# Kernel optimization log

Measured on AMD Instinct MI355X. Metric: run time of the kernel, lower is better.

## Reference

```python
import jax, jax.numpy as jnp
import numpy as np

N = 4096
M0 = 2048
M1 = 2048
MCS = 4096
STRIDE = 2
D_NNGP = STRIDE ** 2 * M1              # 8192, input dim of layer-1 arccos maps
D_NTK = STRIDE ** 2 * (MCS + M1)       # 24576, input dim1 of layer-1 count sketch


def setup_inputs() -> dict:
    key = jax.random.key(0)
    ks = jax.random.split(key, 8)
    return {
        "layer_idx": 1,
        "z_nngp": jax.random.normal(ks[0], (N, D_NNGP), jnp.float32),
        "z_ntk": jax.random.normal(ks[1], (N, D_NTK), jnp.float32),
        "W0": jax.random.normal(ks[2], (D_NNGP, M0), jnp.float32),   # arccos0[1].W
        "W1": jax.random.normal(ks[3], (D_NNGP, M1), jnp.float32),   # arccos1[1].W
        "sign1": (jax.random.randint(ks[4], (D_NTK,), 0, 2) * 2 - 1).astype(jnp.float32),
        "indx1": jax.random.randint(ks[5], (D_NTK,), 0, MCS),
        "sign2": (jax.random.randint(ks[6], (M0,), 0, 2) * 2 - 1).astype(jnp.float32),
        "indx2": jax.random.randint(ks[7], (M0,), 0, MCS),
    }


def count_sketch(x, indx, sign, out_dim):
    # x: [n, d_in]; sign-multiply then scatter_add along last axis into out_dim bins
    xs = x * sign[None, :]
    out = jnp.zeros((x.shape[0], out_dim), dtype=x.dtype)
    return out.at[:, indx].add(xs)


def reference(layer_idx, z_nngp, z_ntk, W0, W1, sign1, indx1, sign2, indx2):
    norm0 = np.sqrt(2.0 / M0).astype(np.float32)
    norm1 = np.float32(np.sqrt(2.0 / M1) / 2.0)
    # arccos order-0 feature map (step function)
    xw0 = z_nngp @ W0
    tmp = (xw0 > 0).astype(z_nngp.dtype) * norm0          # [N, M0]
    # arccos order-1 feature map (relu-like: |xw| + xw)
    xw1 = z_nngp @ W1
    z_nngp_out = (jnp.abs(xw1) + xw1) * norm1             # [N, M1]
    # tensor sketch: count-sketch both, FFT, complex pointwise multiply, ifft.real
    x_cs = count_sketch(z_ntk, indx1, sign1, MCS)         # [N, MCS]
    y_cs = count_sketch(tmp, indx2, sign2, MCS)           # [N, MCS]
    z_ntk_out = jnp.fft.ifft(jnp.fft.fft(x_cs, axis=-1) * jnp.fft.fft(y_cs, axis=-1)).real
    z_ntk_cat = jnp.concatenate([z_nngp_out, z_ntk_out], axis=1)  # [N, M1+MCS]
    return (z_nngp_out, z_ntk_cat)
```

## Files before the change

### kernel.cpp

```cpp
#include <hip/hip_runtime.h>

#define NROW 4096
#define KDIM 8192
#define MDIM 2048
#define MCS_ 4096
#define DNTK 24576
#define CATW 6144
#define TAU_HALF 2.5e-3f
#define NT (KDIM / 32)

typedef __attribute__((ext_vector_type(8))) short short8;
typedef __attribute__((ext_vector_type(4))) float f32x4;

__device__ __forceinline__ void split2(float x0, float x1,
                                       unsigned& hi, unsigned& lo) {
    const unsigned u0 = __float_as_uint(x0);
    const unsigned u1 = __float_as_uint(x1);
    hi = (u0 >> 16) | (u1 & 0xFFFF0000u);
    const float l0 = x0 - __uint_as_float(u0 & 0xFFFF0000u);
    const float l1 = x1 - __uint_as_float(u1 & 0xFFFF0000u);
    lo = (__float_as_uint(l0) >> 16) | (__float_as_uint(l1) & 0xFFFF0000u);
}

__device__ __forceinline__ float2 cmulf(float2 a, float2 b) {
    return make_float2(a.x * b.x - a.y * b.y, a.x * b.y + a.y * b.x);
}

__global__ __launch_bounds__(512) void convert_kernel(
    const float* __restrict__ A,
    const float* __restrict__ W1,
    const float* __restrict__ W0,
    short8* __restrict__ aHi, short8* __restrict__ aLo,
    short8* __restrict__ wHi, short8* __restrict__ wLo)
{
    int b = blockIdx.x;
    const int tid = threadIdx.x;
    if (b < 4096) {
        const int P = b >> 8, T = b & 255;
        const float* src = A + (size_t)(P * 256) * KDIM + T * 32;
        short8* dh = aHi + ((size_t)b << 10);
        short8* dl = aLo + ((size_t)b << 10);
        for (int s = tid; s < 1024; s += 512) {
            const int row = ((s >> 6) << 4) | (s & 15);
            const int k0  = ((s >> 4) & 3) * 8;
            const float* p = src + (size_t)row * KDIM + k0;
            const float4 v0 = *reinterpret_cast<const float4*>(p);
            const float4 v1 = *reinterpret_cast<const float4*>(p + 4);
            union { short8 ss; unsigned u[4]; } h, l;
            split2(v0.x, v0.y, h.u[0], l.u[0]);
            split2(v0.z, v0.w, h.u[1], l.u[1]);
            split2(v1.x, v1.y, h.u[2], l.u[2]);
            split2(v1.z, v1.w, h.u[3], l.u[3]);
            dh[s] = h.ss; dl[s] = l.ss;
        }
    } else {
        b -= 4096;
        const int mat = b >> 11;
        const int T   = b & 255;
        const int Pc  = (b >> 8) & 7;
        const float* Wm = mat ? W0 : W1;
        const float* src = Wm + (size_t)(T * 32) * MDIM + Pc * 256;
        short8* dh = wHi + ((size_t)b << 10);
        short8* dl = wLo + ((size_t)b << 10);
        for (int s = tid; s < 1024; s += 512) {
            const int col = ((s >> 6) << 4) | (s & 15);
            const int k0  = ((s >> 4) & 3) * 8;
            float v[8];
#pragma unroll
            for (int j = 0; j < 8; ++j)
                v[j] = src[(size_t)(k0 + j) * MDIM + col];
            union { short8 ss; unsigned u[4]; } h, l;
            split2(v[0], v[1], h.u[0], l.u[0]);
            split2(v[2], v[3], h.u[1], l.u[1]);
            split2(v[4], v[5], h.u[2], l.u[2]);
            split2(v[6], v[7], h.u[3], l.u[3]);
            dh[s] = h.ss; dl[s] = l.ss;
        }
    }
}

__global__ __launch_bounds__(512, 2) void gemm_mfma_pre(
    const short8* __restrict__ aHi, const short8* __restrict__ aLo,
    const short8* __restrict__ wHi, const short8* __restrict__ wLo,
    float* __restrict__ out0, float* __restrict__ outCat)
{
    const int mode = blockIdx.z;
    __shared__ short8 AhiS[2][1024], AloS[2][1024];
    __shared__ short8 BhiS[2][1024], BloS[2][1024];

    const int tid  = threadIdx.x;
    const int lane = tid & 63;
    const int wid  = tid >> 6;
    const int wr   = wid >> 1;
    const int wc   = wid & 1;
    const int brow = blockIdx.y * 256;
    const int bcol = blockIdx.x * 256;

    const size_t aBase = ((size_t)blockIdx.y) << 18;
    const size_t wBase = ((size_t)(mode * 8 + blockIdx.x)) << 18;

    f32x4 acc[4][8];
#pragma unroll
    for (int m = 0; m < 4; ++m)
#pragma unroll
        for (int n = 0; n < 8; ++n)
#pragma unroll
            for (int i = 0; i < 4; ++i) acc[m][n][i] = 0.f;

    short8 st[8];

#define ISSUE(T)                                                             \
    {                                                                        \
        const size_t o = ((size_t)(T)) << 10;                                \
        st[0] = aHi[aBase + o + tid];  st[1] = aHi[aBase + o + tid + 512];   \
        st[2] = aLo[aBase + o + tid];  st[3] = aLo[aBase + o + tid + 512];   \
        st[4] = wHi[wBase + o + tid];  st[5] = wHi[wBase + o + tid + 512];   \
        st[6] = wLo[wBase + o + tid];  st[7] = wLo[wBase + o + tid + 512];   \
    }
#define WRITE(BUF)                                                           \
    {                                                                        \
        AhiS[BUF][tid] = st[0];  AhiS[BUF][tid + 512] = st[1];               \
        AloS[BUF][tid] = st[2];  AloS[BUF][tid + 512] = st[3];               \
        BhiS[BUF][tid] = st[4];  BhiS[BUF][tid + 512] = st[5];               \
        BloS[BUF][tid] = st[6];  BloS[BUF][tid + 512] = st[7];               \
    }

    ISSUE(0); WRITE(0); ISSUE(1);
    __syncthreads();

    for (int t = 0; t < NT; ++t) {
        const int cur = t & 1;

        short8 ah[4], al[4];
#pragma unroll
        for (int m = 0; m < 4; ++m) {
            ah[m] = AhiS[cur][(wr * 4 + m) * 64 + lane];
            al[m] = AloS[cur][(wr * 4 + m) * 64 + lane];
        }

        if (t + 1 < NT) {
            WRITE(cur ^ 1);
            if (t + 2 < NT) ISSUE(t + 2);
        }

#pragma unroll
        for (int n = 0; n < 8; ++n) {
            const short8 bh = BhiS[cur][(wc * 8 + n) * 64 + lane];
            const short8 bl = BloS[cur][(wc * 8 + n) * 64 + lane];
#pragma unroll
            for (int m = 0; m < 4; ++m) {
                acc[m][n] = __builtin_amdgcn_mfma_f32_16x16x32_bf16(
                    ah[m], bh, acc[m][n], 0, 0, 0);
                acc[m][n] = __builtin_amdgcn_mfma_f32_16x16x32_bf16(
                    ah[m], bl, acc[m][n], 0, 0, 0);
                acc[m][n] = __builtin_amdgcn_mfma_f32_16x16x32_bf16(
                    al[m], bh, acc[m][n], 0, 0, 0);
            }
        }
        __syncthreads();
    }
#undef ISSUE
#undef WRITE

    const float norm0 = 0.03125f;
    const int ocol0 = bcol + wc * 128 + (lane & 15);
    const int orow0 = brow + wr * 64 + ((lane >> 4) << 2);
#pragma unroll
    for (int m = 0; m < 4; ++m)
#pragma unroll
        for (int n = 0; n < 8; ++n) {
            const int col = ocol0 + n * 16;
#pragma unroll
            for (int i = 0; i < 4; ++i) {
                const int row = orow0 + m * 16 + i;
                if (mode == 0) {
                    const float v = fmaxf(acc[m][n][i], 0.f) * norm0;
                    out0[(size_t)row * MDIM + col] = v;
                    outCat[(size_t)row * CATW + col] = v;
                } else {
                    outCat[(size_t)row * CATW + 2048 + col] = acc[m][n][i];
                }
            }
        }
}

__global__ __launch_bounds__(512, 2) void gemm_mfma(
    const float* __restrict__ A,
    const float* __restrict__ W1,
    const float* __restrict__ W0,
    float* __restrict__ out0,
    float* __restrict__ outCat)
{
    const int mode = blockIdx.z;
    const float* __restrict__ W = mode ? W0 : W1;

    __shared__ short8 AhiS[2][1024], AloS[2][1024];
    __shared__ short8 BhiS[2][1024], BloS[2][1024];

    const int tid  = threadIdx.x;
    const int lane = tid & 63;
    const int wid  = tid >> 6;
    const int wr   = wid >> 1;
    const int wc   = wid & 1;
    const int brow = blockIdx.y * 256;
    const int bcol = blockIdx.x * 256;

    f32x4 acc[4][8];
#pragma unroll
    for (int m = 0; m < 4; ++m)
#pragma unroll
        for (int n = 0; n < 8; ++n)
#pragma unroll
            for (int i = 0; i < 4; ++i) acc[m][n][i] = 0.f;

    const int srow  = tid >> 1;
    const int skh   = tid & 1;
    const int slot0 = (srow >> 4) * 64 + (srow & 15) + (skh << 5);
    const float* aptr = A + (size_t)(brow + srow) * KDIM + skh * 16;
    const float* bptr = W + (size_t)(skh * 16) * MDIM + (bcol + srow);

    float4 av0, av1, av2, av3;
    float  bst[16];

#define LOAD_TILE(T)                                                         \
    {                                                                        \
        const float* ap = aptr + (T) * 32;                                   \
        av0 = *reinterpret_cast<const float4*>(ap);                          \
        av1 = *reinterpret_cast<const float4*>(ap + 4);                      \
        av2 = *reinterpret_cast<const float4*>(ap + 8);                      \
        av3 = *reinterpret_cast<const float4*>(ap + 12);                     \
        const float* bp = bptr + (size_t)((T) * 32) * MDIM;                  \
        _Pragma("unroll")                                                    \
        for (int j = 0; j < 16; ++j) bst[j] = bp[(size_t)j * MDIM];          \
    }
#define CONVERT_WRITE(BUF)                                                   \
    {                                                                        \
        union { short8 s; unsigned u[4]; } h, l;                             \
        split2(av0.x, av0.y, h.u[0], l.u[0]);                                \
        split2(av0.z, av0.w, h.u[1], l.u[1]);                                \
        split2(av1.x, av1.y, h.u[2], l.u[2]);                                \
        split2(av1.z, av1.w, h.u[3], l.u[3]);                                \
        AhiS[BUF][slot0] = h.s;  AloS[BUF][slot0] = l.s;                     \
        split2(av2.x, av2.y, h.u[0], l.u[0]);                                \
        split2(av2.z, av2.w, h.u[1], l.u[1]);                                \
        split2(av3.x, av3.y, h.u[2], l.u[2]);                                \
        split2(av3.z, av3.w, h.u[3], l.u[3]);                                \
        AhiS[BUF][slot0 + 16] = h.s;  AloS[BUF][slot0 + 16] = l.s;           \
        split2(bst[0], bst[1], h.u[0], l.u[0]);                              \
        split2(bst[2], bst[3], h.u[1], l.u[1]);                              \
        split2(bst[4], bst[5], h.u[2], l.u[2]);                              \
        split2(bst[6], bst[7], h.u[3], l.u[3]);                              \
        BhiS[BUF][slot0] = h.s;  BloS[BUF][slot0] = l.s;                     \
        split2(bst[8],  bst[9],  h.u[0], l.u[0]);                            \
        split2(bst[10], bst[11], h.u[1], l.u[1]);                            \
        split2(bst[12], bst[13], h.u[2], l.u[2]);                            \
        split2(bst[14], bst[15], h.u[3], l.u[3]);                            \
        BhiS[BUF][slot0 + 16] = h.s;  BloS[BUF][slot0 + 16] = l.s;           \
    }

    LOAD_TILE(0);
    CONVERT_WRITE(0);
    LOAD_TILE(1);
    __syncthreads();

    for (int t = 0; t < NT; ++t) {
        const int cur = t & 1;
        short8 ah[4], al[4];
#pragma unroll
        for (int m = 0; m < 4; ++m) {
            ah[m] = AhiS[cur][(wr * 4 + m) * 64 + lane];
            al[m] = AloS[cur][(wr * 4 + m) * 64 + lane];
        }
        if (t + 1 < NT) {
            CONVERT_WRITE(cur ^ 1);
            if (t + 2 < NT) LOAD_TILE(t + 2);
        }
#pragma unroll
        for (int n = 0; n < 8; ++n) {
            const short8 bh = BhiS[cur][(wc * 8 + n) * 64 + lane];
            const short8 bl = BloS[cur][(wc * 8 + n) * 64 + lane];
#pragma unroll
            for (int m = 0; m < 4; ++m) {
                acc[m][n] = __builtin_amdgcn_mfma_f32_16x16x32_bf16(
                    ah[m], bh, acc[m][n], 0, 0, 0);
                acc[m][n] = __builtin_amdgcn_mfma_f32_16x16x32_bf16(
                    ah[m], bl, acc[m][n], 0, 0, 0);
                acc[m][n] = __builtin_amdgcn_mfma_f32_16x16x32_bf16(
                    al[m], bh, acc[m][n], 0, 0, 0);
            }
        }
        __syncthreads();
    }
#undef LOAD_TILE
#undef CONVERT_WRITE

    const float norm0 = 0.03125f;
    const int ocol0 = bcol + wc * 128 + (lane & 15);
    const int orow0 = brow + wr * 64 + ((lane >> 4) << 2);
#pragma unroll
    for (int m = 0; m < 4; ++m)
#pragma unroll
        for (int n = 0; n < 8; ++n) {
            const int col = ocol0 + n * 16;
#pragma unroll
            for (int i = 0; i < 4; ++i) {
                const int row = orow0 + m * 16 + i;
                if (mode == 0) {
                    const float v = fmaxf(acc[m][n][i], 0.f) * norm0;
                    out0[(size_t)row * MDIM + col] = v;
                    outCat[(size_t)row * CATW + col] = v;
                } else {
                    outCat[(size_t)row * CATW + 2048 + col] = acc[m][n][i];
                }
            }
        }
}

#define ZP(i) Z[(i) + ((i) >> 4)]
#define YBASE 4608

__device__ __forceinline__ float2 twfetch(const float2* RT, int t) {
    if (t <= 512) return RT[t];
    const float2 r = RT[1024 - t];
    return make_float2(-r.y, -r.x);
}

__global__ __launch_bounds__(512) void sketch_fft_kernel(
    const float* __restrict__ z_ntk,
    const float* __restrict__ sign1,
    const int*   __restrict__ indx1,
    const float* __restrict__ sign2,
    const int*   __restrict__ indx2,
    float* __restrict__ outCat)
{
    __shared__ float2 Z[4352];
    __shared__ float2 RT[513];
    float* Zf = reinterpret_cast<float*>(Z);
    const int tid = threadIdx.x;
    const int row = blockIdx.x;

    for (int i = tid; i < 2176; i += 512)
        reinterpret_cast<float4*>(Zf)[i] = make_float4(0.f, 0.f, 0.f, 0.f);
    const float wconst = -1.5339807878856412e-3f;
    for (int t = tid; t <= 512; t += 512) {
        float sw, cw;
        __sincosf(wconst * (float)t, &sw, &cw);
        RT[t] = make_float2(cw, sw);
    }
    __syncthreads();

    const float4* xrow4 = reinterpret_cast<const float4*>(z_ntk + (size_t)row * DNTK);
    const float4* s1v   = reinterpret_cast<const float4*>(sign1);
    const int4*   i1v   = reinterpret_cast<const int4*>(indx1);
    for (int c = 0; c < 12; c += 4) {
        float4 xs[4], ss[4]; int4 iv[4];
#pragma unroll
        for (int j = 0; j < 4; ++j) {
            const int v = tid + (c + j) * 512;
            xs[j] = xrow4[v]; ss[j] = s1v[v]; iv[j] = i1v[v];
        }
#pragma unroll
        for (int j = 0; j < 4; ++j) {
            atomicAdd(&Zf[iv[j].x], xs[j].x * ss[j].x);
            atomicAdd(&Zf[iv[j].y], xs[j].y * ss[j].y);
            atomicAdd(&Zf[iv[j].z], xs[j].z * ss[j].z);
            atomicAdd(&Zf[iv[j].w], xs[j].w * ss[j].w);
        }
    }
    const float norm0 = 0.03125f;
    const float* trow = outCat + (size_t)row * CATW + 2048;
    {
        const float4 t4 = reinterpret_cast<const float4*>(trow)[tid];
        const float4 s  = reinterpret_cast<const float4*>(sign2)[tid];
        const int4   ix = reinterpret_cast<const int4*>(indx2)[tid];
        const float y0 = (fabsf(t4.x) < TAU_HALF) ? 0.5f * norm0 : (t4.x > 0.f ? norm0 : 0.f);
        const float y1 = (fabsf(t4.y) < TAU_HALF) ? 0.5f * norm0 : (t4.y > 0.f ? norm0 : 0.f);
        const float y2 = (fabsf(t4.z) < TAU_HALF) ? 0.5f * norm0 : (t4.z > 0.f ? norm0 : 0.f);
        const float y3 = (fabsf(t4.w) < TAU_HALF) ? 0.5f * norm0 : (t4.w > 0.f ? norm0 : 0.f);
        atomicAdd(&Zf[YBASE + ix.x], y0 * s.x);
        atomicAdd(&Zf[YBASE + ix.y], y1 * s.y);
        atomicAdd(&Zf[YBASE + ix.z], y2 * s.z);
        atomicAdd(&Zf[YBASE + ix.w], y3 * s.w);
    }
    __syncthreads();

    {
        float re[8], im[8];
#pragma unroll
        for (int j = 0; j < 8; ++j) {
            const int i = tid + j * 512;
            re[j] = Zf[i];
            im[j] = Zf[YBASE + i];
        }
        __syncthreads();
#pragma unroll
        for (int j = 0; j < 8; ++j) {
            const int i = tid + j * 512;
            ZP(i) = make_float2(re[j], im[j]);
        }
    }
    __syncthreads();

#pragma unroll
    for (int s = 0; s < 6; ++s) {
        const int lq = 2 * (5 - s);
        const int q  = 1 << lq;
        for (int b = tid; b < 1024; b += 512) {
            const int j    = b & (q - 1);
            const int base = ((b >> lq) << (lq + 2)) + j;
            const float2 x0 = ZP(base);
            const float2 x1 = ZP(base + q);
            const float2 x2 = ZP(base + 2 * q);
            const float2 x3 = ZP(base + 3 * q);
            const float2 w1 = twfetch(RT, j << (10 - lq));
            const float2 w2 = cmulf(w1, w1);
            const float2 w3 = cmulf(w2, w1);
            const float2 sA = make_float2(x0.x + x2.x, x0.y + x2.y);
            const float2 sB = make_float2(x0.x - x2.x, x0.y - x2.y);
            const float2 sC = make_float2(x1.x + x3.x, x1.y + x3.y);
            const float2 sD = make_float2(x1.x - x3.x, x1.y - x3.y);
            ZP(base) = make_float2(sA.x + sC.x, sA.y + sC.y);
            const float2 u1 = make_float2(sB.x + sD.y, sB.y - sD.x);
            const float2 u2 = make_float2(sA.x - sC.x, sA.y - sC.y);
            const float2 u3 = make_float2(sB.x - sD.y, sB.y + sD.x);
            ZP(base + q)     = cmulf(u1, w1);
            ZP(base + 2 * q) = cmulf(u2, w2);
            ZP(base + 3 * q) = cmulf(u3, w3);
        }
        __syncthreads();
    }

    for (int p = tid; p < MCS_; p += 512) {
        int q;
        if (p == 0) q = 0;
        else { const int h = 31 - __clz(p); q = 5 * (1 << (h & ~1)) - 1 - p; }
        if (p <= q) {
            const float2 Ap = ZP(p);
            const float2 Bq = ZP(q);
            const float Xr = 0.5f * (Ap.x + Bq.x);
            const float Xi = 0.5f * (Ap.y - Bq.y);
            const float Yr = 0.5f * (Ap.y + Bq.y);
            const float Yi = -0.5f * (Ap.x - Bq.x);
            const float Pr = Xr * Yr - Xi * Yi;
            const float Pi = Xr * Yi + Xi * Yr;
            ZP(p) = make_float2(Pr, Pi);
            ZP(q) = make_float2(Pr, -Pi);
        }
    }
    __syncthreads();

#pragma unroll
    for (int s = 0; s < 6; ++s) {
        const int lq = 2 * s;
        const int q  = 1 << lq;
        for (int b = tid; b < 1024; b += 512) {
            const int j    = b & (q - 1);
            const int base = ((b >> lq) << (lq + 2)) + j;
            const float2 t1 = twfetch(RT, j << (10 - lq));
            const float2 w1 = make_float2(t1.x, -t1.y);
            const float2 w2 = cmulf(w1, w1);
            const float2 w3 = cmulf(w2, w1);
            const float2 a  = ZP(base);
            const float2 b1 = cmulf(ZP(base + q),     w1);
            const float2 c  = cmulf(ZP(base + 2 * q), w2);
            const float2 d  = cmulf(ZP(base + 3 * q), w3);
            const float2 sA = make_float2(a.x + c.x, a.y + c.y);
            const float2 sB = make_float2(a.x - c.x, a.y - c.y);
            const float2 sC = make_float2(b1.x + d.x, b1.y + d.y);
            const float2 sD = make_float2(b1.x - d.x, b1.y - d.y);
            ZP(base)         = make_float2(sA.x + sC.x, sA.y + sC.y);
            ZP(base + q)     = make_float2(sB.x - sD.y, sB.y + sD.x);
            ZP(base + 2 * q) = make_float2(sA.x - sC.x, sA.y - sC.y);
            ZP(base + 3 * q) = make_float2(sB.x + sD.y, sB.y - sD.x);
        }
        __syncthreads();
    }

    float* orow = outCat + (size_t)row * CATW + 2048;
    const float scale = 1.0f / (float)MCS_;
    for (int n = tid; n < MCS_; n += 512) orow[n] = ZP(n).x * scale;
}

extern "C" void kernel_launch(void* const* d_in, const int* in_sizes, int n_in,
                              void* d_out, int out_size, void* d_ws, size_t ws_size,
                              hipStream_t stream) {
    (void)in_sizes; (void)n_in; (void)out_size;
    const float* z_nngp = (const float*)d_in[1];
    const float* z_ntk  = (const float*)d_in[2];
    const float* W0     = (const float*)d_in[3];
    const float* W1     = (const float*)d_in[4];
    const float* sign1  = (const float*)d_in[5];
    const int*   indx1  = (const int*)d_in[6];
    const float* sign2  = (const float*)d_in[7];
    const int*   indx2  = (const int*)d_in[8];

    float* out0   = (float*)d_out;
    float* outCat = out0 + (size_t)NROW * MDIM;

    const size_t NEED = 268435456ull;
    if (ws_size >= NEED) {
        short8* aHi = (short8*)d_ws;
        short8* aLo = aHi + (1ull << 22);
        short8* wHi = aLo + (1ull << 22);
        short8* wLo = wHi + (1ull << 22);
        convert_kernel<<<dim3(8192), dim3(512), 0, stream>>>(
            z_nngp, W1, W0, aHi, aLo, wHi, wLo);
        gemm_mfma_pre<<<dim3(8, 16, 2), dim3(512), 0, stream>>>(
            aHi, aLo, wHi, wLo, out0, outCat);
    } else {
        gemm_mfma<<<dim3(8, 16, 2), dim3(512), 0, stream>>>(
            z_nngp, W1, W0, out0, outCat);
    }

    sketch_fft_kernel<<<dim3(NROW), dim3(512), 0, stream>>>(
        z_ntk, sign1, indx1, sign2, indx2, outCat);
}
```

Measured before the change: 1.291 ms.

## Replace LDS atomic count-sketch scatter with CSR gather per bin

Adds a small kernel that builds CSR bucket lists (sorted by source index, with the sign packed into the high bit) for both count sketches. The per-row sketch+FFT kernel then stages the z_ntk row in LDS in chunks and has each thread gather-accumulate its 8 bins in registers, avoiding contended LDS float atomics. The cost is an extra serial build kernel with an insertion sort, irregular per-thread work, and more global reads of the entry lists and syncs per row.

New measurement: 1.275 ms. About the same (-1.2%).

```diff
diff --git a/kernel.cpp b/kernel.cpp
--- a/kernel.cpp
+++ b/kernel.cpp
@@ -79,6 +79,68 @@
     }
 }
 
+__global__ __launch_bounds__(512) void csr_build(
+    const int* __restrict__ indx1, const float* __restrict__ sign1,
+    const int* __restrict__ indx2, const float* __restrict__ sign2,
+    int* __restrict__ rowptr1, int* __restrict__ ent1,
+    int* __restrict__ rowptr2, int* __restrict__ ent2)
+{
+    const int which = blockIdx.x;
+    const int*   idx = which ? indx2 : indx1;
+    const float* sg  = which ? sign2 : sign1;
+    const int    n   = which ? 2048 : 24576;
+    int* rowptr = which ? rowptr2 : rowptr1;
+    int* ent    = which ? ent2 : ent1;
+
+    __shared__ int h[4096];
+    __shared__ int rp[4097];
+    __shared__ int part[512];
+    const int tid = threadIdx.x;
+
+    for (int i = tid; i < 4096; i += 512) h[i] = 0;
+    __syncthreads();
+    for (int d = tid; d < n; d += 512) atomicAdd(&h[idx[d]], 1);
+    __syncthreads();
+
+    int loc[8], s = 0;
+#pragma unroll
+    for (int k = 0; k < 8; ++k) { loc[k] = h[8 * tid + k]; s += loc[k]; }
+    part[tid] = s;
+    __syncthreads();
+    for (int off = 1; off < 512; off <<= 1) {
+        int v = part[tid];
+        if (tid >= off) v += part[tid - off];
+        __syncthreads();
+        part[tid] = v;
+        __syncthreads();
+    }
+    int base = tid ? part[tid - 1] : 0;
+#pragma unroll
+    for (int k = 0; k < 8; ++k) { rp[8 * tid + k] = base; base += loc[k]; }
+    if (tid == 511) rp[4096] = base;
+    __syncthreads();
+
+    for (int i = tid; i < 4096; i += 512) h[i] = 0;
+    __syncthreads();
+    for (int d = tid; d < n; d += 512) {
+        const int b   = idx[d];
+        const int pos = atomicAdd(&h[b], 1);
+        ent[rp[b] + pos] = d | (sg[d] < 0.f ? 0x80000000 : 0);
+    }
+    __syncthreads();
+
+    for (int i = tid; i < 4097; i += 512) rowptr[i] = rp[i];
+    for (int b = tid; b < 4096; b += 512) {
+        const int lo = rp[b], hi = rp[b + 1];
+        for (int i = lo + 1; i < hi; ++i) {
+            const int e = ent[i], key = e & 0x7FFFFFFF;
+            int j = i - 1;
+            while (j >= lo && (ent[j] & 0x7FFFFFFF) > key) { ent[j + 1] = ent[j]; --j; }
+            ent[j + 1] = e;
+        }
+    }
+}
+
 __global__ __launch_bounds__(512, 2) void gemm_mfma_pre(
     const short8* __restrict__ aHi, const short8* __restrict__ aLo,
     const short8* __restrict__ wHi, const short8* __restrict__ wLo,
@@ -317,7 +379,6 @@
 }
 
 #define ZP(i) Z[(i) + ((i) >> 4)]
-#define YBASE 4608
 
 __device__ __forceinline__ float2 twfetch(const float2* RT, int t) {
     if (t <= 512) return RT[t];
@@ -325,82 +386,7 @@
     return make_float2(-r.y, -r.x);
 }
 
-__global__ __launch_bounds__(512) void sketch_fft_kernel(
-    const float* __restrict__ z_ntk,
-    const float* __restrict__ sign1,
-    const int*   __restrict__ indx1,
-    const float* __restrict__ sign2,
-    const int*   __restrict__ indx2,
-    float* __restrict__ outCat)
-{
-    __shared__ float2 Z[4352];
-    __shared__ float2 RT[513];
-    float* Zf = reinterpret_cast<float*>(Z);
-    const int tid = threadIdx.x;
-    const int row = blockIdx.x;
-
-    for (int i = tid; i < 2176; i += 512)
-        reinterpret_cast<float4*>(Zf)[i] = make_float4(0.f, 0.f, 0.f, 0.f);
-    const float wconst = -1.5339807878856412e-3f;
-    for (int t = tid; t <= 512; t += 512) {
-        float sw, cw;
-        __sincosf(wconst * (float)t, &sw, &cw);
-        RT[t] = make_float2(cw, sw);
-    }
-    __syncthreads();
-
-    const float4* xrow4 = reinterpret_cast<const float4*>(z_ntk + (size_t)row * DNTK);
-    const float4* s1v   = reinterpret_cast<const float4*>(sign1);
-    const int4*   i1v   = reinterpret_cast<const int4*>(indx1);
-    for (int c = 0; c < 12; c += 4) {
-        float4 xs[4], ss[4]; int4 iv[4];
-#pragma unroll
-        for (int j = 0; j < 4; ++j) {
-            const int v = tid + (c + j) * 512;
-            xs[j] = xrow4[v]; ss[j] = s1v[v]; iv[j] = i1v[v];
-        }
-#pragma unroll
-        for (int j = 0; j < 4; ++j) {
-            atomicAdd(&Zf[iv[j].x], xs[j].x * ss[j].x);
-            atomicAdd(&Zf[iv[j].y], xs[j].y * ss[j].y);
-            atomicAdd(&Zf[iv[j].z], xs[j].z * ss[j].z);
-            atomicAdd(&Zf[iv[j].w], xs[j].w * ss[j].w);
-        }
-    }
-    const float norm0 = 0.03125f;
-    const float* trow = outCat + (size_t)row * CATW + 2048;
-    {
-        const float4 t4 = reinterpret_cast<const float4*>(trow)[tid];
-        const float4 s  = reinterpret_cast<const float4*>(sign2)[tid];
-        const int4   ix = reinterpret_cast<const int4*>(indx2)[tid];
-        const float y0 = (fabsf(t4.x) < TAU_HALF) ? 0.5f * norm0 : (t4.x > 0.f ? norm0 : 0.f);
-        const float y1 = (fabsf(t4.y) < TAU_HALF) ? 0.5f * norm0 : (t4.y > 0.f ? norm0 : 0.f);
-        const float y2 = (fabsf(t4.z) < TAU_HALF) ? 0.5f * norm0 : (t4.z > 0.f ? norm0 : 0.f);
-        const float y3 = (fabsf(t4.w) < TAU_HALF) ? 0.5f * norm0 : (t4.w > 0.f ? norm0 : 0.f);
-        atomicAdd(&Zf[YBASE + ix.x], y0 * s.x);
-        atomicAdd(&Zf[YBASE + ix.y], y1 * s.y);
-        atomicAdd(&Zf[YBASE + ix.z], y2 * s.z);
-        atomicAdd(&Zf[YBASE + ix.w], y3 * s.w);
-    }
-    __syncthreads();
-
-    {
-        float re[8], im[8];
-#pragma unroll
-        for (int j = 0; j < 8; ++j) {
-            const int i = tid + j * 512;
-            re[j] = Zf[i];
-            im[j] = Zf[YBASE + i];
-        }
-        __syncthreads();
-#pragma unroll
-        for (int j = 0; j < 8; ++j) {
-            const int i = tid + j * 512;
-            ZP(i) = make_float2(re[j], im[j]);
-        }
-    }
-    __syncthreads();
-
+__device__ __forceinline__ void fft_conv_body(float2* Z, const float2* RT, int tid) {
 #pragma unroll
     for (int s = 0; s < 6; ++s) {
         const int lq = 2 * (5 - s);
@@ -475,6 +461,165 @@
         }
         __syncthreads();
     }
+}
+
+__global__ __launch_bounds__(512) void sketch_fft_csr(
+    const float* __restrict__ z_ntk,
+    const int* __restrict__ rowptr1, const int* __restrict__ ent1,
+    const int* __restrict__ rowptr2, const int* __restrict__ ent2,
+    float* __restrict__ outCat)
+{
+    __shared__ __align__(16) float2 Z[4352];
+    __shared__ float2 RT[513];
+    float* Zf = reinterpret_cast<float*>(Z);
+    const int tid = threadIdx.x;
+    const int row = blockIdx.x;
+    const float norm0 = 0.03125f;
+
+    const float wconst = -1.5339807878856412e-3f;
+    for (int t = tid; t <= 512; t += 512) {
+        float sw, cw;
+        __sincosf(wconst * (float)t, &sw, &cw);
+        RT[t] = make_float2(cw, sw);
+    }
+
+    int rpx[9], rpy[9];
+#pragma unroll
+    for (int k = 0; k < 9; ++k) {
+        rpx[k] = rowptr1[8 * tid + k];
+        rpy[k] = rowptr2[8 * tid + k];
+    }
+    float accX[8], accY[8];
+#pragma unroll
+    for (int k = 0; k < 8; ++k) { accX[k] = 0.f; accY[k] = 0.f; }
+    int cur[8];
+#pragma unroll
+    for (int k = 0; k < 8; ++k) cur[k] = rpx[k];
+
+    const float4* xrow4 = reinterpret_cast<const float4*>(z_ntk + (size_t)row * DNTK);
+    for (int c = 0; c < 3; ++c) {
+        const int lo = c * 8192, hi = lo + 8192;
+        __syncthreads();
+#pragma unroll
+        for (int j = 0; j < 4; ++j)
+            reinterpret_cast<float4*>(Zf)[tid + j * 512] = xrow4[c * 2048 + tid + j * 512];
+        __syncthreads();
+#pragma unroll
+        for (int k = 0; k < 8; ++k) {
+            while (cur[k] < rpx[k + 1]) {
+                const int e = ent1[cur[k]];
+                const int d = e & 0x7FFFFFFF;
+                if (d >= hi) break;
+                const float v = Zf[d - lo];
+                accX[k] += (e < 0) ? -v : v;
+                ++cur[k];
+            }
+        }
+    }
+
+    const float* trow = outCat + (size_t)row * CATW + 2048;
+    __syncthreads();
+    reinterpret_cast<float4*>(Zf)[tid] = reinterpret_cast<const float4*>(trow)[tid];
+    __syncthreads();
+#pragma unroll
+    for (int k = 0; k < 8; ++k) {
+        for (int c = rpy[k]; c < rpy[k + 1]; ++c) {
+            const int e = ent2[c];
+            const int d = e & 0x7FFFFFFF;
+            const float t = Zf[d];
+            const float y = (fabsf(t) < TAU_HALF) ? 0.5f * norm0
+                                                  : (t > 0.f ? norm0 : 0.f);
+            accY[k] += (e < 0) ? -y : y;
+        }
+    }
+    __syncthreads();
+
+#pragma unroll
+    for (int k = 0; k < 8; ++k) {
+        const int b = 8 * tid + k;
+        ZP(b) = make_float2(accX[k], accY[k]);
+    }
+    __syncthreads();
+
+    fft_conv_body(Z, RT, tid);
+
+    float* orow = outCat + (size_t)row * CATW + 2048;
+    const float scale = 1.0f / (float)MCS_;
+    for (int n = tid; n < MCS_; n += 512) orow[n] = ZP(n).x * scale;
+}
+
+#define YBASE 4608
+__global__ __launch_bounds__(512) void sketch_fft_atomic(
+    const float* __restrict__ z_ntk,
+    const float* __restrict__ sign1,
+    const int*   __restrict__ indx1,
+    const float* __restrict__ sign2,
+    const int*   __restrict__ indx2,
+    float* __restrict__ outCat)
+{
+    __shared__ __align__(16) float2 Z[4352];
+    __shared__ float2 RT[513];
+    float* Zf = reinterpret_cast<float*>(Z);
+    const int tid = threadIdx.x;
+    const int row = blockIdx.x;
+
+    for (int i = tid; i < 2176; i += 512)
+        reinterpret_cast<float4*>(Zf)[i] = make_float4(0.f, 0.f, 0.f, 0.f);
+    const float wconst = -1.5339807878856412e-3f;
+    for (int t = tid; t <= 512; t += 512) {
+        float sw, cw;
+        __sincosf(wconst * (float)t, &sw, &cw);
+        RT[t] = make_float2(cw, sw);
+    }
+    __syncthreads();
+
+    const float4* xrow4 = reinterpret_cast<const float4*>(z_ntk + (size_t)row * DNTK);
+    const float4* s1v   = reinterpret_cast<const float4*>(sign1);
+    const int4*   i1v   = reinterpret_cast<const int4*>(indx1);
+    for (int v = tid; v < DNTK / 4; v += 512) {
+        const float4 x = xrow4[v];
+        const float4 s = s1v[v];
+        const int4   ix = i1v[v];
+        atomicAdd(&Zf[ix.x], x.x * s.x);
+        atomicAdd(&Zf[ix.y], x.y * s.y);
+        atomicAdd(&Zf[ix.z], x.z * s.z);
+        atomicAdd(&Zf[ix.w], x.w * s.w);
+    }
+    const float norm0 = 0.03125f;
+    const float* trow = outCat + (size_t)row * CATW + 2048;
+    {
+        const float4 t4 = reinterpret_cast<const float4*>(trow)[tid];
+        const float4 s  = reinterpret_cast<const float4*>(sign2)[tid];
+        const int4   ix = reinterpret_cast<const int4*>(indx2)[tid];
+        const float y0 = (fabsf(t4.x) < TAU_HALF) ? 0.5f * norm0 : (t4.x > 0.f ? norm0 : 0.f);
+        const float y1 = (fabsf(t4.y) < TAU_HALF) ? 0.5f * norm0 : (t4.y > 0.f ? norm0 : 0.f);
+        const float y2 = (fabsf(t4.z) < TAU_HALF) ? 0.5f * norm0 : (t4.z > 0.f ? norm0 : 0.f);
+        const float y3 = (fabsf(t4.w) < TAU_HALF) ? 0.5f * norm0 : (t4.w > 0.f ? norm0 : 0.f);
+        atomicAdd(&Zf[YBASE + ix.x], y0 * s.x);
+        atomicAdd(&Zf[YBASE + ix.y], y1 * s.y);
+        atomicAdd(&Zf[YBASE + ix.z], y2 * s.z);
+        atomicAdd(&Zf[YBASE + ix.w], y3 * s.w);
+    }
+    __syncthreads();
+
+    {
+        float re[8], im[8];
+#pragma unroll
+        for (int j = 0; j < 8; ++j) {
+            const int i = tid + j * 512;
+            re[j] = Zf[i];
+            im[j] = Zf[YBASE + i];
+        }
+        __syncthreads();
+#pragma unroll
+        for (int j = 0; j < 8; ++j) {
+            const int i = tid + j * 512;
+            ZP(i) = make_float2(re[j], im[j]);
+        }
+    }
+    __syncthreads();
+
+    fft_conv_body(Z, RT, tid);
 
     float* orow = outCat + (size_t)row * CATW + 2048;
     const float scale = 1.0f / (float)MCS_;
@@ -497,8 +642,23 @@
     float* out0   = (float*)d_out;
     float* outCat = out0 + (size_t)NROW * MDIM;
 
-    const size_t NEED = 268435456ull;
-    if (ws_size >= NEED) {
+    const size_t NEED_P = 268435456ull;
+    const size_t NEED_C = NEED_P + (1ull << 20);
+
+    int* rowptr1 = nullptr; int* rowptr2 = nullptr;
+    int* ent1 = nullptr;    int* ent2 = nullptr;
+    const bool csr_ok = ws_size >= NEED_C;
+    if (csr_ok) {
+        int* base = (int*)((char*)d_ws + NEED_P);
+        rowptr1 = base;
+        rowptr2 = base + 4352;
+        ent1    = base + 8704;
+        ent2    = ent1 + 24576;
+        csr_build<<<dim3(2), dim3(512), 0, stream>>>(
+            indx1, sign1, indx2, sign2, rowptr1, ent1, rowptr2, ent2);
+    }
+
+    if (ws_size >= NEED_P) {
         short8* aHi = (short8*)d_ws;
         short8* aLo = aHi + (1ull << 22);
         short8* wHi = aLo + (1ull << 22);
@@ -512,6 +672,11 @@
             z_nngp, W1, W0, out0, outCat);
     }
 
-    sketch_fft_kernel<<<dim3(NROW), dim3(512), 0, stream>>>(
-        z_ntk, sign1, indx1, sign2, indx2, outCat);
-}
+    if (csr_ok) {
+        sketch_fft_csr<<<dim3(NROW), dim3(512), 0, stream>>>(
+            z_ntk, rowptr1, ent1, rowptr2, ent2, outCat);
+    } else {
+        sketch_fft_atomic<<<dim3(NROW), dim3(512), 0, stream>>>(
+            z_ntk, sign1, indx1, sign2, indx2, outCat);
+    }
+}
```
